# Optimization experiments

Measured on AMD Instinct MI355X. Metric: run time of the kernel, lower is better.

## Reference

```python
import jax, jax.numpy as jnp
import numpy as np

N_SRC = 50000
N_EDGES = 150000
D_IN = 512
D_OUT = 512

def setup_inputs() -> dict:
    key = jax.random.key(0)
    k1, k2, k3, k4, k5 = jax.random.split(key, 5)
    src_h = jax.random.normal(k1, (N_SRC, D_IN), dtype=jnp.float32)
    W = jax.random.normal(k2, (D_OUT, D_IN), dtype=jnp.float32) * (1.0 / np.sqrt(D_IN))
    b = jax.random.normal(k3, (D_OUT,), dtype=jnp.float32) * 0.01
    src_idx = jax.random.randint(k4, (N_EDGES,), 0, N_SRC, dtype=jnp.int64) if jax.config.jax_enable_x64 else jax.random.randint(k4, (N_EDGES,), 0, N_SRC, dtype=jnp.int32)
    dst_idx = jax.random.randint(k5, (N_EDGES,), 0, N_SRC, dtype=src_idx.dtype)
    return {"src_h": src_h, "W": W, "b": b, "src_idx": src_idx, "dst_idx": dst_idx, "n_dst": N_SRC}

def reference(src_h, W, b, src_idx, dst_idx, n_dst):
    # message passing: copy src feature to each edge, sum into dst nodes
    msgs = src_h[src_idx]                                  # [E, D_in]
    agg = jax.ops.segment_sum(msgs, dst_idx, num_segments=n_dst)  # [N_dst, D_in]
    # dense linear (apply_linear == 'linear' -> no relu)
    return agg @ W.T + b                                   # [N_dst, D_out]
```

## Files before the change

kernel.cpp:

```cpp
#include <hip/hip_runtime.h>
#include <hip/hip_bf16.h>

#define D 512
#define BM 128
#define BN 128
#define BK 32
#define SB 512

typedef __attribute__((ext_vector_type(8))) short bf16x8;
typedef __attribute__((ext_vector_type(4))) float f32x4;

__device__ __forceinline__ unsigned short bf16_rne(float f) {
    union { float f; unsigned u; } v; v.f = f;
    return (unsigned short)((v.u + 0x7FFFu + ((v.u >> 16) & 1u)) >> 16);
}

__device__ __forceinline__ void gload16(const void* g, void* l) {
    __builtin_amdgcn_global_load_lds(
        (const __attribute__((address_space(1))) void*)g,
        (__attribute__((address_space(3))) void*)l,
        16, 0, 0);
}


__global__ __launch_bounds__(256) void hist_kernel(const int* __restrict__ dst, int E,
                                                   int* __restrict__ cnt) {
    int e = blockIdx.x * 256 + threadIdx.x;
    if (e < E) atomicAdd(&cnt[dst[e]], 1);
}

__global__ __launch_bounds__(256) void scan_reduce_kernel(const int* __restrict__ cnt, int M,
                                                          int* __restrict__ bsum) {
    const int t = threadIdx.x;
    const int i0 = blockIdx.x * SB + t * 2;
    int v = 0;
    if (i0 < M)     v += cnt[i0];
    if (i0 + 1 < M) v += cnt[i0 + 1];
    #pragma unroll
    for (int o = 32; o > 0; o >>= 1) v += __shfl_down(v, o, 64);
    __shared__ int ws_[4];
    if ((t & 63) == 0) ws_[t >> 6] = v;
    __syncthreads();
    if (t == 0) bsum[blockIdx.x] = ws_[0] + ws_[1] + ws_[2] + ws_[3];
}

__global__ __launch_bounds__(256) void scan_bsum_kernel(const int* __restrict__ bsum, int NB,
                                                        int* __restrict__ bscan,
                                                        int* __restrict__ offsets, int M) {
    __shared__ int s[256];
    const int t = threadIdx.x;
    int v = (t < NB) ? bsum[t] : 0;
    s[t] = v;
    __syncthreads();
    #pragma unroll
    for (int o = 1; o < 256; o <<= 1) {
        int u = (t >= o) ? s[t - o] : 0;
        __syncthreads();
        s[t] += u;
        __syncthreads();
    }
    if (t < NB) bscan[t] = s[t] - v;
    if (t == 255) offsets[M] = s[255];
}

__global__ __launch_bounds__(256) void scan_final_kernel(int* __restrict__ cnt, int M,
                                                         const int* __restrict__ bscan,
                                                         int* __restrict__ offsets) {
    __shared__ int s[256];
    const int t = threadIdx.x;
    const int base = blockIdx.x * SB + t * 2;
    int a = (base < M) ? cnt[base] : 0;
    int b = (base + 1 < M) ? cnt[base + 1] : 0;
    const int tsum = a + b;
    s[t] = tsum;
    __syncthreads();
    #pragma unroll
    for (int o = 1; o < 256; o <<= 1) {
        int u = (t >= o) ? s[t - o] : 0;
        __syncthreads();
        s[t] += u;
        __syncthreads();
    }
    const int excl = s[t] - tsum + bscan[blockIdx.x];
    if (base < M)     { offsets[base] = excl;         cnt[base] = excl; }
    if (base + 1 < M) { offsets[base + 1] = excl + a; cnt[base + 1] = excl + a; }
}

__global__ __launch_bounds__(256) void sort_kernel(const int* __restrict__ src,
                                                   const int* __restrict__ dst, int E,
                                                   int* __restrict__ cursor,
                                                   int* __restrict__ sorted_src) {
    int e = blockIdx.x * 256 + threadIdx.x;
    if (e < E) {
        int pos = atomicAdd(&cursor[dst[e]], 1);
        sorted_src[pos] = src[e];
    }
}


__global__ __launch_bounds__(128) void agg_kernel(const float* __restrict__ src_h,
                                                  const int* __restrict__ offsets,
                                                  const int* __restrict__ sorted_src,
                                                  unsigned short* __restrict__ aggb) {
    const int d = blockIdx.x;
    const int t = threadIdx.x;
    const int beg = offsets[d];
    const int end = offsets[d + 1];
    float4 acc = {0.f, 0.f, 0.f, 0.f};
    for (int e = beg; e < end; ++e) {
        const int s = sorted_src[e];
        float4 v = ((const float4*)(src_h + (size_t)s * D))[t];
        acc.x += v.x; acc.y += v.y; acc.z += v.z; acc.w += v.w;
    }
    ushort4 o;
    o.x = bf16_rne(acc.x); o.y = bf16_rne(acc.y);
    o.z = bf16_rne(acc.z); o.w = bf16_rne(acc.w);
    *(ushort4*)(aggb + (size_t)d * D + t * 4) = o;
}


__global__ __launch_bounds__(256) void wconv_kernel(const float* __restrict__ W,
                                                    unsigned short* __restrict__ wb) {
    int i = blockIdx.x * 256 + threadIdx.x;
    float2 v = ((const float2*)W)[i];
    unsigned r = ((unsigned)bf16_rne(v.x)) | (((unsigned)bf16_rne(v.y)) << 16);
    ((unsigned*)wb)[i] = r;
}


__global__ __launch_bounds__(256) void gemm_kernel(const unsigned short* __restrict__ A,
                                                   const unsigned short* __restrict__ B,
                                                   const float* __restrict__ bias,
                                                   float* __restrict__ out,
                                                   int M, int MB_tiles) {
    __shared__ __align__(16) unsigned short As[BM * BK];
    __shared__ __align__(16) unsigned short Bs[BN * BK];

    const int L = blockIdx.x;
    const int mb = (L >> 5) * 8 + (L & 7);
    const int nb = (L >> 3) & 3;
    if (mb >= MB_tiles) return;
    const int m0 = mb * BM;
    const int n0 = nb * BN;

    const int t = threadIdx.x;
    const int lane = t & 63;
    const int wave = t >> 6;
    const int wm = wave >> 1;
    const int wn = wave & 1;
    const int quad = lane >> 4;
    const int lr = lane & 15;

    const int srow = t >> 2;
    const int scol = ((t & 3) ^ ((t >> 3) & 3)) * 8;
    const int arow0 = min(m0 + srow, M - 1);
    const int arow1 = min(m0 + 64 + srow, M - 1);
    const int brow0 = n0 + srow;
    const int brow1 = n0 + 64 + srow;

    const int fsw = (quad ^ ((lr >> 1) & 3)) * 8;

    f32x4 acc[4][4] = {};

    for (int k0 = 0; k0 < D; k0 += BK) {
        gload16(A + (size_t)arow0 * D + k0 + scol, As + t * 8);
        gload16(A + (size_t)arow1 * D + k0 + scol, As + 2048 + t * 8);
        gload16(B + (size_t)brow0 * D + k0 + scol, Bs + t * 8);
        gload16(B + (size_t)brow1 * D + k0 + scol, Bs + 2048 + t * 8);
        __syncthreads();

        bf16x8 af[4], bfr[4];
        #pragma unroll
        for (int i = 0; i < 4; ++i) {
            af[i]  = *(const bf16x8*)&As[(wm * 64 + i * 16 + lr) * BK + fsw];
            bfr[i] = *(const bf16x8*)&Bs[(wn * 64 + i * 16 + lr) * BK + fsw];
        }
        #pragma unroll
        for (int i = 0; i < 4; ++i)
            #pragma unroll
            for (int j = 0; j < 4; ++j)
                acc[i][j] = __builtin_amdgcn_mfma_f32_16x16x32_bf16(af[i], bfr[j], acc[i][j], 0, 0, 0);
        __syncthreads();
    }

    #pragma unroll
    for (int j = 0; j < 4; ++j) {
        const int col = n0 + wn * 64 + j * 16 + lr;
        const float bv = bias[col];
        #pragma unroll
        for (int i = 0; i < 4; ++i) {
            const int rbase = m0 + wm * 64 + i * 16 + quad * 4;
            #pragma unroll
            for (int r = 0; r < 4; ++r) {
                const int row = rbase + r;
                if (row < M) out[(size_t)row * D + col] = acc[i][j][r] + bv;
            }
        }
    }
}

extern "C" void kernel_launch(void* const* d_in, const int* in_sizes, int n_in,
                              void* d_out, int out_size, void* d_ws, size_t ws_size,
                              hipStream_t stream) {
    const float* src_h = (const float*)d_in[0];
    const float* W     = (const float*)d_in[1];
    const float* b     = (const float*)d_in[2];
    const int*   si    = (const int*)d_in[3];
    const int*   di    = (const int*)d_in[4];
    const int M = in_sizes[0] / D;
    const int E = in_sizes[3];
    const int NB = (M + SB - 1) / SB;

    char* ws = (char*)d_ws;
    unsigned short* aggb = (unsigned short*)ws;
    unsigned short* wb   = (unsigned short*)(ws + 51200000);
    int* offsets         = (int*)(ws + 51724288);
    int* cnt             = (int*)(ws + 51924480);
    int* ssrc            = (int*)(ws + 52124480);
    int* bsum            = (int*)(ws + 52724480);
    int* bscan           = (int*)(ws + 52726480);

    hipMemsetAsync(cnt, 0, (size_t)M * sizeof(int), stream);
    wconv_kernel<<<dim3((D * D / 2) / 256), 256, 0, stream>>>(W, wb);
    hist_kernel<<<dim3((E + 255) / 256), 256, 0, stream>>>(di, E, cnt);
    scan_reduce_kernel<<<dim3(NB), 256, 0, stream>>>(cnt, M, bsum);
    scan_bsum_kernel<<<1, 256, 0, stream>>>(bsum, NB, bscan, offsets, M);
    scan_final_kernel<<<dim3(NB), 256, 0, stream>>>(cnt, M, bscan, offsets);
    sort_kernel<<<dim3((E + 255) / 256), 256, 0, stream>>>(si, di, E, cnt, ssrc);
    agg_kernel<<<dim3(M), 128, 0, stream>>>(src_h, offsets, ssrc, aggb);

    const int MB_tiles = (M + BM - 1) / BM;
    const int ngrid = ((MB_tiles + 7) / 8) * 32;
    gemm_kernel<<<dim3(ngrid), 256, 0, stream>>>(aggb, wb, b, (float*)d_out, M, MB_tiles);
}
```

Before: 317.6 us.

## Merge W conversion into histogram kernel and use wave-per-node unrolled aggregation

Fuses the weight bf16 conversion and the destination histogram into one launch, removing a kernel launch. Reworks aggregation so each 64-lane wavefront handles one destination node (four per block), with each lane covering two float4 chunks and edges unrolled by four to keep more independent gather loads in flight. This targets latency-bound row gathers and per-block overhead from launching one small block per node. It adds more register use and remainder-handling code.

```diff
diff --git a/kernel.cpp b/kernel.cpp
--- a/kernel.cpp
+++ b/kernel.cpp
@@ -22,12 +22,27 @@
         16, 0, 0);
 }
 
-
-__global__ __launch_bounds__(256) void hist_kernel(const int* __restrict__ dst, int E,
+__device__ __forceinline__ void facc(float4& a, const float4 v) {
+    a.x += v.x; a.y += v.y; a.z += v.z; a.w += v.w;
+}
+
+__global__ __launch_bounds__(256) void prep_kernel(const float* __restrict__ W,
+                                                   unsigned short* __restrict__ wb,
+                                                   const int* __restrict__ dst, int E,
                                                    int* __restrict__ cnt) {
-    int e = blockIdx.x * 256 + threadIdx.x;
-    if (e < E) atomicAdd(&cnt[dst[e]], 1);
-}
+    const int b = blockIdx.x;
+    const int t = threadIdx.x;
+    if (b < 512) {
+        const int i = b * 256 + t;
+        float2 v = ((const float2*)W)[i];
+        unsigned r = ((unsigned)bf16_rne(v.x)) | (((unsigned)bf16_rne(v.y)) << 16);
+        ((unsigned*)wb)[i] = r;
+    } else {
+        const int e = (b - 512) * 256 + t;
+        if (e < E) atomicAdd(&cnt[dst[e]], 1);
+    }
+}
+
 
 __global__ __launch_bounds__(256) void scan_reduce_kernel(const int* __restrict__ cnt, int M,
                                                           int* __restrict__ bsum) {
@@ -97,34 +112,66 @@
     }
 }
 
-
-__global__ __launch_bounds__(128) void agg_kernel(const float* __restrict__ src_h,
+__global__ __launch_bounds__(256) void agg_kernel(const float* __restrict__ src_h,
                                                   const int* __restrict__ offsets,
                                                   const int* __restrict__ sorted_src,
-                                                  unsigned short* __restrict__ aggb) {
-    const int d = blockIdx.x;
-    const int t = threadIdx.x;
+                                                  unsigned short* __restrict__ aggb,
+                                                  int M) {
+    const int wv = threadIdx.x >> 6;
+    const int lane = threadIdx.x & 63;
+    const int d = blockIdx.x * 4 + wv;
+    if (d >= M) return;
     const int beg = offsets[d];
     const int end = offsets[d + 1];
-    float4 acc = {0.f, 0.f, 0.f, 0.f};
-    for (int e = beg; e < end; ++e) {
-        const int s = sorted_src[e];
-        float4 v = ((const float4*)(src_h + (size_t)s * D))[t];
-        acc.x += v.x; acc.y += v.y; acc.z += v.z; acc.w += v.w;
-    }
-    ushort4 o;
-    o.x = bf16_rne(acc.x); o.y = bf16_rne(acc.y);
-    o.z = bf16_rne(acc.z); o.w = bf16_rne(acc.w);
-    *(ushort4*)(aggb + (size_t)d * D + t * 4) = o;
-}
-
-
-__global__ __launch_bounds__(256) void wconv_kernel(const float* __restrict__ W,
-                                                    unsigned short* __restrict__ wb) {
-    int i = blockIdx.x * 256 + threadIdx.x;
-    float2 v = ((const float2*)W)[i];
-    unsigned r = ((unsigned)bf16_rne(v.x)) | (((unsigned)bf16_rne(v.y)) << 16);
-    ((unsigned*)wb)[i] = r;
+    const float4* rb = (const float4*)src_h;
+
+    float4 a0 = {0.f, 0.f, 0.f, 0.f};
+    float4 a1 = {0.f, 0.f, 0.f, 0.f};
+    int e = beg;
+
+    for (; e + 4 <= end; e += 4) {
+        const int s0 = sorted_src[e];
+        const int s1 = sorted_src[e + 1];
+        const int s2 = sorted_src[e + 2];
+        const int s3 = sorted_src[e + 3];
+        float4 v00 = rb[(size_t)s0 * 128 + lane];
+        float4 v01 = rb[(size_t)s0 * 128 + 64 + lane];
+        float4 v10 = rb[(size_t)s1 * 128 + lane];
+        float4 v11 = rb[(size_t)s1 * 128 + 64 + lane];
+        float4 v20 = rb[(size_t)s2 * 128 + lane];
+        float4 v21 = rb[(size_t)s2 * 128 + 64 + lane];
+        float4 v30 = rb[(size_t)s3 * 128 + lane];
+        float4 v31 = rb[(size_t)s3 * 128 + 64 + lane];
+        facc(a0, v00); facc(a1, v01);
+        facc(a0, v10); facc(a1, v11);
+        facc(a0, v20); facc(a1, v21);
+        facc(a0, v30); facc(a1, v31);
+    }
+    if (e + 2 <= end) {
+        const int s0 = sorted_src[e];
+        const int s1 = sorted_src[e + 1];
+        float4 v00 = rb[(size_t)s0 * 128 + lane];
+        float4 v01 = rb[(size_t)s0 * 128 + 64 + lane];
+        float4 v10 = rb[(size_t)s1 * 128 + lane];
+        float4 v11 = rb[(size_t)s1 * 128 + 64 + lane];
+        facc(a0, v00); facc(a1, v01);
+        facc(a0, v10); facc(a1, v11);
+        e += 2;
+    }
+    if (e < end) {
+        const int s0 = sorted_src[e];
+        float4 v00 = rb[(size_t)s0 * 128 + lane];
+        float4 v01 = rb[(size_t)s0 * 128 + 64 + lane];
+        facc(a0, v00); facc(a1, v01);
+    }
+
+    ushort4 o0, o1;
+    o0.x = bf16_rne(a0.x); o0.y = bf16_rne(a0.y);
+    o0.z = bf16_rne(a0.z); o0.w = bf16_rne(a0.w);
+    o1.x = bf16_rne(a1.x); o1.y = bf16_rne(a1.y);
+    o1.z = bf16_rne(a1.z); o1.w = bf16_rne(a1.w);
+    *(ushort4*)(aggb + (size_t)d * D + lane * 4) = o0;
+    *(ushort4*)(aggb + (size_t)d * D + 256 + lane * 4) = o1;
 }
 
 
@@ -221,13 +268,13 @@
     int* bscan           = (int*)(ws + 52726480);
 
     hipMemsetAsync(cnt, 0, (size_t)M * sizeof(int), stream);
-    wconv_kernel<<<dim3((D * D / 2) / 256), 256, 0, stream>>>(W, wb);
-    hist_kernel<<<dim3((E + 255) / 256), 256, 0, stream>>>(di, E, cnt);
+    const int HB = (E + 255) / 256;
+    prep_kernel<<<dim3(512 + HB), 256, 0, stream>>>(W, wb, di, E, cnt);
     scan_reduce_kernel<<<dim3(NB), 256, 0, stream>>>(cnt, M, bsum);
     scan_bsum_kernel<<<1, 256, 0, stream>>>(bsum, NB, bscan, offsets, M);
     scan_final_kernel<<<dim3(NB), 256, 0, stream>>>(cnt, M, bscan, offsets);
     sort_kernel<<<dim3((E + 255) / 256), 256, 0, stream>>>(si, di, E, cnt, ssrc);
-    agg_kernel<<<dim3(M), 128, 0, stream>>>(src_h, offsets, ssrc, aggb);
+    agg_kernel<<<dim3((M + 3) / 4), 256, 0, stream>>>(src_h, offsets, ssrc, aggb, M);
 
     const int MB_tiles = (M + BM - 1) / BM;
     const int ngrid = ((MB_tiles + 7) / 8) * 32;
```

Result: faster. 310.0 us (-2.4%).
